# Performance work log

Hardware: AMD Instinct MI355X
Metric: run time of the kernel (lower is better)

Reference implementation:

```python
import jax, jax.numpy as jnp
import numpy as np

N = 50000
F_IN = 128
HID = 64
HEADS = 4
CLASSES = 16
E = 800000
NEG_SLOPE = 0.2


def _gat_layer(x, src, dst, W, a_src, a_dst, bias, heads, ch, concat):
    n = x.shape[0]
    h = (x @ W).reshape(n, heads, ch)                     # [N,H,C]
    alpha_src = jnp.einsum('nhc,hc->nh', h, a_src)        # [N,H]
    alpha_dst = jnp.einsum('nhc,hc->nh', h, a_dst)        # [N,H]
    e = jax.nn.leaky_relu(alpha_src[src] + alpha_dst[dst], NEG_SLOPE)  # [E,H]
    # segment softmax over edges grouped by destination node
    m = jax.ops.segment_max(e, dst, num_segments=n)       # [N,H]
    ex = jnp.exp(e - m[dst])                              # [E,H]
    s = jax.ops.segment_sum(ex, dst, num_segments=n)      # [N,H]
    alpha = ex / (s[dst] + 1e-16)                         # [E,H]
    # weighted scatter-add aggregation of neighbor features
    out = jax.ops.segment_sum(h[src] * alpha[:, :, None], dst, num_segments=n)  # [N,H,C]
    if concat:
        return out.reshape(n, heads * ch) + bias
    return out.mean(axis=1) + bias


def setup_inputs() -> dict:
    key = jax.random.key(0)
    ks = jax.random.split(key, 12)
    x = jax.random.normal(ks[0], (N, F_IN), dtype=jnp.float32)
    edge_index = jax.random.randint(ks[1], (2, E), 0, N, dtype=jnp.int64)
    g1 = 1.0 / np.sqrt(F_IN)
    g2 = 1.0 / np.sqrt(HID * HEADS)
    W1 = jax.random.normal(ks[2], (F_IN, HEADS * HID), dtype=jnp.float32) * g1
    a_src1 = jax.random.normal(ks[3], (HEADS, HID), dtype=jnp.float32) * g1
    a_dst1 = jax.random.normal(ks[4], (HEADS, HID), dtype=jnp.float32) * g1
    b1 = jnp.zeros((HEADS * HID,), dtype=jnp.float32)
    W2 = jax.random.normal(ks[5], (HEADS * HID, CLASSES), dtype=jnp.float32) * g2
    a_src2 = jax.random.normal(ks[6], (1, CLASSES), dtype=jnp.float32) * g2
    a_dst2 = jax.random.normal(ks[7], (1, CLASSES), dtype=jnp.float32) * g2
    b2 = jnp.zeros((CLASSES,), dtype=jnp.float32)
    return {"x": x, "edge_index": edge_index, "W1": W1, "a_src1": a_src1,
            "a_dst1": a_dst1, "b1": b1, "W2": W2, "a_src2": a_src2,
            "a_dst2": a_dst2, "b2": b2}


def reference(x, edge_index, W1, a_src1, a_dst1, b1, W2, a_src2, a_dst2, b2):
    n = x.shape[0]
    # add self-loops (PyG GATConv default add_self_loops=True)
    loops = jnp.arange(n, dtype=edge_index.dtype)
    src = jnp.concatenate([edge_index[0], loops])
    dst = jnp.concatenate([edge_index[1], loops])
    h = _gat_layer(x, src, dst, W1, a_src1, a_dst1, b1, HEADS, HID, concat=True)
    h = jax.nn.elu(h)
    out = _gat_layer(h, src, dst, W2, a_src2, a_dst2, b2, 1, CLASSES, concat=False)
    return jax.nn.log_softmax(out, axis=1)
```

## Files before the change

### kernel.cpp

```cpp
#include <hip/hip_runtime.h>
#include <hip/hip_fp16.h>
#include <math.h>

#define NEG 0.2f

typedef __attribute__((ext_vector_type(8))) short bf16x8;
typedef __attribute__((ext_vector_type(4))) float f32x4;

__device__ __forceinline__ float lrelu(float x){ return x > 0.f ? x : NEG*x; }

__device__ __forceinline__ float bflo(unsigned u){ return __uint_as_float(u << 16); }
__device__ __forceinline__ float bfhi(unsigned u){ return __uint_as_float(u & 0xffff0000u); }

__device__ __forceinline__ float selh(float a0, float a1, float a2, float a3,
                                      bool bit0, bool bit1){
  float lo = bit0 ? a1 : a0;
  float hi = bit0 ? a3 : a2;
  return bit1 ? hi : lo;
}

__device__ __forceinline__ unsigned short f2bf(float x){
  unsigned u = __float_as_uint(x);
  u += 0x7fffu + ((u >> 16) & 1u);
  return (unsigned short)(u >> 16);
}

#define FMA8(e, h) \
  acc[0]=fmaf(e,bflo(h.x),acc[0]); acc[1]=fmaf(e,bfhi(h.x),acc[1]); \
  acc[2]=fmaf(e,bflo(h.y),acc[2]); acc[3]=fmaf(e,bfhi(h.y),acc[3]); \
  acc[4]=fmaf(e,bflo(h.z),acc[4]); acc[5]=fmaf(e,bfhi(h.z),acc[5]); \
  acc[6]=fmaf(e,bflo(h.w),acc[6]); acc[7]=fmaf(e,bfhi(h.w),acc[7]);

__global__ void fill_kernel(const int* __restrict__ ei,
                            int* __restrict__ cnt, int* __restrict__ adj, int E){
  __shared__ int s_is64;
  if (threadIdx.x < 64){
    int v = ei[2*threadIdx.x + 1];
    unsigned long long b = __ballot(v != 0);
    if (threadIdx.x == 0) s_is64 = (b == 0ULL) ? 1 : 0;
  }
  __syncthreads();
  int is64 = s_is64;
  int stride = gridDim.x * blockDim.x;
  for (int i = blockIdx.x*blockDim.x + threadIdx.x; i < E; i += stride){
    int s = is64 ? ei[2*i]       : ei[i];
    int d = is64 ? ei[2*(E + i)] : ei[E + i];
    int pos = atomicAdd(&cnt[d], 1);
    if (pos < 64) adj[(d << 6) + pos] = s;
  }
}

__device__ __forceinline__ int wt_addr(int col, int k){
  int g = (k >> 3) ^ (col & 7);
  return col*128 + g*8 + (k & 7);
}

__global__ __launch_bounds__(256) void gemm1_mfma(const float* __restrict__ x,
                             const float* __restrict__ W,
                             const float* __restrict__ asrcw, const float* __restrict__ adstw,
                             unsigned short* __restrict__ h1b,
                             float* __restrict__ as1, float* __restrict__ ad1, int N){
  __shared__ unsigned short wt[256*128];
  int t = threadIdx.x;
  int lane = t & 63, w = t >> 6;
  int row0 = blockIdx.x * 64 + w * 16;

  int arow = row0 + (lane & 15);
  if (arow >= N) arow = N - 1;
  const float* xr = x + (size_t)arow * 128 + (lane >> 4) * 8;
  bf16x8 afrag[4];
  #pragma unroll
  for (int kk = 0; kk < 4; kk++){
    float4 p0 = *reinterpret_cast<const float4*>(xr + kk*32);
    float4 p1 = *reinterpret_cast<const float4*>(xr + kk*32 + 4);
    afrag[kk][0] = (short)f2bf(p0.x); afrag[kk][1] = (short)f2bf(p0.y);
    afrag[kk][2] = (short)f2bf(p0.z); afrag[kk][3] = (short)f2bf(p0.w);
    afrag[kk][4] = (short)f2bf(p1.x); afrag[kk][5] = (short)f2bf(p1.y);
    afrag[kk][6] = (short)f2bf(p1.z); afrag[kk][7] = (short)f2bf(p1.w);
  }

  int c = t;
  for (int k0 = 0; k0 < 128; k0 += 8){
    bf16x8 v;
    #pragma unroll
    for (int j = 0; j < 8; j++) v[j] = (short)f2bf(W[(size_t)(k0+j)*256 + c]);
    *reinterpret_cast<bf16x8*>(&wt[wt_addr(c, k0)]) = v;
  }
  __syncthreads();

  f32x4 acc[16];
  #pragma unroll
  for (int n = 0; n < 16; n++) acc[n] = (f32x4){0.f,0.f,0.f,0.f};
  #pragma unroll
  for (int kk = 0; kk < 4; kk++){
    #pragma unroll
    for (int n = 0; n < 16; n++){
      bf16x8 b = *reinterpret_cast<const bf16x8*>(
          &wt[wt_addr(n*16 + (lane & 15), kk*32 + (lane >> 4)*8)]);
      acc[n] = __builtin_amdgcn_mfma_f32_16x16x32_bf16(afrag[kk], b, acc[n], 0, 0, 0);
    }
  }

  int rbase = row0 + (lane >> 4)*4;
  int cbase = lane & 15;
  #pragma unroll
  for (int n = 0; n < 16; n++){
    #pragma unroll
    for (int r = 0; r < 4; r++){
      int row = rbase + r;
      if (row < N) h1b[(size_t)row*256 + n*16 + cbase] = f2bf(acc[n][r]);
    }
  }

  float av[16], dv[16];
  #pragma unroll
  for (int n = 0; n < 16; n++){
    av[n] = asrcw[n*16 + cbase];
    dv[n] = adstw[n*16 + cbase];
  }
  #pragma unroll
  for (int r = 0; r < 4; r++){
    int row = rbase + r;
    float hs[4], hd[4];
    #pragma unroll
    for (int h = 0; h < 4; h++){
      float ps = 0.f, pd = 0.f;
      #pragma unroll
      for (int q = 0; q < 4; q++){
        int n = h*4 + q;
        ps = fmaf(acc[n][r], av[n], ps);
        pd = fmaf(acc[n][r], dv[n], pd);
      }
      #pragma unroll
      for (int off = 1; off < 16; off <<= 1){
        ps += __shfl_xor(ps, off, 64);
        pd += __shfl_xor(pd, off, 64);
      }
      hs[h] = ps; hd[h] = pd;
    }
    if (cbase == 0 && row < N){
      *reinterpret_cast<float4*>(as1 + (size_t)row*4) = make_float4(hs[0],hs[1],hs[2],hs[3]);
      *reinterpret_cast<float4*>(ad1 + (size_t)row*4) = make_float4(hd[0],hd[1],hd[2],hd[3]);
    }
  }
}

__global__ void edge_exp_kernel(const float* __restrict__ as1, const float* __restrict__ ad1,
                                const int* __restrict__ cnt, const int* __restrict__ adj,
                                __half* __restrict__ exarr, float* __restrict__ den, int N){
  int node = (blockIdx.x*blockDim.x + threadIdx.x) >> 6;
  int lane = threadIdx.x & 63;
  if (node >= N) return;
  int cn = cnt[node]; if (cn > 64) cn = 64;
  int beg = node << 6;
  bool val = lane < cn;
  int src = val ? adj[beg + lane] : 0;
  float4 dv = *reinterpret_cast<const float4*>(ad1 + (size_t)node*4);
  float4 sv = *reinterpret_cast<const float4*>(as1 + (size_t)src*4);
  float ex0 = val ? __expf(lrelu(sv.x + dv.x)) : 0.f;
  float ex1 = val ? __expf(lrelu(sv.y + dv.y)) : 0.f;
  float ex2 = val ? __expf(lrelu(sv.z + dv.z)) : 0.f;
  float ex3 = val ? __expf(lrelu(sv.w + dv.w)) : 0.f;

  if (val){
    __half2 p0 = __floats2half2_rn(ex0, ex1);
    __half2 p1 = __floats2half2_rn(ex2, ex3);
    uint2 o;
    o.x = *reinterpret_cast<unsigned*>(&p0);
    o.y = *reinterpret_cast<unsigned*>(&p1);
    *reinterpret_cast<uint2*>(exarr + (size_t)(beg + lane)*4) = o;
  }

  float sp0 = ex0, sp1 = ex1, sp2 = ex2, sp3 = ex3;
  #pragma unroll
  for (int off = 32; off; off >>= 1){
    sp0 += __shfl_xor(sp0, off, 64);
    sp1 += __shfl_xor(sp1, off, 64);
    sp2 += __shfl_xor(sp2, off, 64);
    sp3 += __shfl_xor(sp3, off, 64);
  }
  float4 s2 = *reinterpret_cast<const float4*>(as1 + (size_t)node*4);
  float exs0 = __expf(lrelu(s2.x + dv.x));
  float exs1 = __expf(lrelu(s2.y + dv.y));
  float exs2 = __expf(lrelu(s2.z + dv.z));
  float exs3 = __expf(lrelu(s2.w + dv.w));
  if (lane == 0){
    *reinterpret_cast<float4*>(den + (size_t)node*8) =
        make_float4(sp0 + exs0, sp1 + exs1, sp2 + exs2, sp3 + exs3);
    *reinterpret_cast<float4*>(den + (size_t)node*8 + 4) =
        make_float4(exs0, exs1, exs2, exs3);
  }
}

__global__ void agg1_kernel(const unsigned short* __restrict__ h1b,
                            const float* __restrict__ b1,
                            const int* __restrict__ cnt, const int* __restrict__ adj,
                            const __half* __restrict__ exarr, const float* __restrict__ den,
                            unsigned short* __restrict__ hact_b, int N){
  int node = (blockIdx.x*blockDim.x + threadIdx.x) >> 6;
  int lane = threadIdx.x & 63;
  if (node >= N) return;
  int cn = cnt[node]; if (cn > 64) cn = 64;
  int beg = node << 6;
  int hf = lane >> 5;
  int sl = lane & 31;
  int hh = sl >> 3;
  bool hb0 = (sl & 8) != 0, hb1 = (sl & 16) != 0;
  const __half* exw = exarr + (size_t)beg*4;
  const int* aj = adj + beg;
  unsigned co = sl*8;

  float acc[8];
  #pragma unroll
  for (int q = 0; q < 8; q++) acc[q] = 0.f;

  int j = 0;
  for (; j + 8 <= cn; j += 8){
    int e0 = j+hf, e1 = j+2+hf, e2 = j+4+hf, e3 = j+6+hf;
    int s0 = aj[e0], s1 = aj[e1], s2 = aj[e2], s3 = aj[e3];
    float w0 = __half2float(exw[e0*4+hh]);
    float w1 = __half2float(exw[e1*4+hh]);
    float w2 = __half2float(exw[e2*4+hh]);
    float w3 = __half2float(exw[e3*4+hh]);
    uint4 h0 = *reinterpret_cast<const uint4*>(h1b + (size_t)s0*256 + co);
    uint4 h1 = *reinterpret_cast<const uint4*>(h1b + (size_t)s1*256 + co);
    uint4 h2 = *reinterpret_cast<const uint4*>(h1b + (size_t)s2*256 + co);
    uint4 h3 = *reinterpret_cast<const uint4*>(h1b + (size_t)s3*256 + co);
    FMA8(w0, h0); FMA8(w1, h1); FMA8(w2, h2); FMA8(w3, h3);
  }
  for (; j + 4 <= cn; j += 4){
    int e0 = j+hf, e1 = j+2+hf;
    int s0 = aj[e0], s1 = aj[e1];
    float w0 = __half2float(exw[e0*4+hh]);
    float w1 = __half2float(exw[e1*4+hh]);
    uint4 h0 = *reinterpret_cast<const uint4*>(h1b + (size_t)s0*256 + co);
    uint4 h1 = *reinterpret_cast<const uint4*>(h1b + (size_t)s1*256 + co);
    FMA8(w0, h0); FMA8(w1, h1);
  }
  for (; j < cn; j += 2){
    if (j + hf < cn){
      int e0 = j+hf;
      int s0 = aj[e0];
      float w0 = __half2float(exw[e0*4+hh]);
      uint4 h0 = *reinterpret_cast<const uint4*>(h1b + (size_t)s0*256 + co);
      FMA8(w0, h0);
    }
  }

  #pragma unroll
  for (int q = 0; q < 8; q++) acc[q] += __shfl_xor(acc[q], 32, 64);

  if (hf == 0){
    float4 dn  = *reinterpret_cast<const float4*>(den + (size_t)node*8);
    float4 dsf = *reinterpret_cast<const float4*>(den + (size_t)node*8 + 4);
    float dh  = selh(dn.x, dn.y, dn.z, dn.w, hb0, hb1);
    float ehs = selh(dsf.x, dsf.y, dsf.z, dsf.w, hb0, hb1);
    uint4 hv = *reinterpret_cast<const uint4*>(h1b + (size_t)node*256 + co);
    FMA8(ehs, hv);

    float rinv = 1.0f / (dh + 1e-16f);
    float4 bA = *reinterpret_cast<const float4*>(b1 + sl*8);
    float4 bB = *reinterpret_cast<const float4*>(b1 + sl*8 + 4);
    float o[8];
    o[0] = acc[0]*rinv + bA.x; o[1] = acc[1]*rinv + bA.y;
    o[2] = acc[2]*rinv + bA.z; o[3] = acc[3]*rinv + bA.w;
    o[4] = acc[4]*rinv + bB.x; o[5] = acc[5]*rinv + bB.y;
    o[6] = acc[6]*rinv + bB.z; o[7] = acc[7]*rinv + bB.w;
    #pragma unroll
    for (int q = 0; q < 8; q++) o[q] = o[q] > 0.f ? o[q] : expm1f(o[q]);
    uint4 ob;
    ob.x = (unsigned)f2bf(o[0]) | ((unsigned)f2bf(o[1]) << 16);
    ob.y = (unsigned)f2bf(o[2]) | ((unsigned)f2bf(o[3]) << 16);
    ob.z = (unsigned)f2bf(o[4]) | ((unsigned)f2bf(o[5]) << 16);
    ob.w = (unsigned)f2bf(o[6]) | ((unsigned)f2bf(o[7]) << 16);
    *reinterpret_cast<uint4*>(hact_b + (size_t)node*256 + co) = ob;
  }
}

__device__ __forceinline__ int wt2_addr(int col, int k){
  int g = (k >> 3) ^ (col & 7);
  return col*256 + g*8 + (k & 7);
}

__global__ __launch_bounds__(256) void gemm2_mfma(const unsigned short* __restrict__ hact_b,
                             const float* __restrict__ W2,
                             const float* __restrict__ asrc2, const float* __restrict__ adst2,
                             float* __restrict__ h2, float* __restrict__ as2,
                             float* __restrict__ ad2, int N){
  __shared__ unsigned short wt[16*256];
  int t = threadIdx.x;
  int lane = t & 63, w = t >> 6;
  int row0 = blockIdx.x * 64 + w * 16;

  {
    float4 r0 = *reinterpret_cast<const float4*>(W2 + (size_t)t*16);
    float4 r1 = *reinterpret_cast<const float4*>(W2 + (size_t)t*16 + 4);
    float4 r2 = *reinterpret_cast<const float4*>(W2 + (size_t)t*16 + 8);
    float4 r3 = *reinterpret_cast<const float4*>(W2 + (size_t)t*16 + 12);
    float wr[16] = {r0.x,r0.y,r0.z,r0.w, r1.x,r1.y,r1.z,r1.w,
                    r2.x,r2.y,r2.z,r2.w, r3.x,r3.y,r3.z,r3.w};
    #pragma unroll
    for (int cc = 0; cc < 16; cc++) wt[wt2_addr(cc, t)] = f2bf(wr[cc]);
  }

  int arow = row0 + (lane & 15);
  if (arow >= N) arow = N - 1;
  const unsigned short* hr = hact_b + (size_t)arow*256 + (lane >> 4)*8;
  __syncthreads();

  f32x4 acc = (f32x4){0.f,0.f,0.f,0.f};
  #pragma unroll
  for (int kk = 0; kk < 8; kk++){
    bf16x8 a = *reinterpret_cast<const bf16x8*>(hr + kk*32);
    bf16x8 b = *reinterpret_cast<const bf16x8*>(
        &wt[wt2_addr(lane & 15, kk*32 + (lane >> 4)*8)]);
    acc = __builtin_amdgcn_mfma_f32_16x16x32_bf16(a, b, acc, 0, 0, 0);
  }

  int rbase = row0 + (lane >> 4)*4;
  int cbase = lane & 15;
  float avc = asrc2[cbase], dvc = adst2[cbase];
  #pragma unroll
  for (int r = 0; r < 4; r++){
    int row = rbase + r;
    if (row < N) h2[(size_t)row*16 + cbase] = acc[r];
    float ps = acc[r]*avc, pd = acc[r]*dvc;
    #pragma unroll
    for (int off = 1; off < 16; off <<= 1){
      ps += __shfl_xor(ps, off, 64);
      pd += __shfl_xor(pd, off, 64);
    }
    if (cbase == 0 && row < N){ as2[row] = ps; ad2[row] = pd; }
  }
}

__global__ void agg2_kernel(const float* __restrict__ h2, const float* __restrict__ as2,
                            const float* __restrict__ ad2, const float* __restrict__ b2,
                            const int* __restrict__ cnt, const int* __restrict__ adj,
                            float* __restrict__ out, int N){
  int node = (blockIdx.x*blockDim.x + threadIdx.x) >> 6;
  int lane = threadIdx.x & 63;
  if (node >= N) return;
  int cn = cnt[node]; if (cn > 64) cn = 64;
  int beg = node << 6;
  int g = lane >> 4, c = lane & 15;

  bool val = lane < cn;
  int srcl = val ? adj[beg + lane] : 0;
  float adn = ad2[node];

  float v[16];
  #pragma unroll
  for (int q = 0; q < 16; q++){
    v[q] = 0.f;
    if (4*q < cn){
      int sj = __shfl(srcl, 4*q + g, 64);
      v[q] = h2[(size_t)sj*16 + c];
    }
  }

  float e = val ? lrelu(as2[srcl] + adn) : -3e38f;
  float ex = __expf(e);
  float sp = ex;
  #pragma unroll
  for (int off = 32; off; off >>= 1) sp += __shfl_xor(sp, off, 64);
  float eself = __expf(lrelu(as2[node] + adn));
  sp += eself;

  float acc = 0.f;
  #pragma unroll
  for (int q = 0; q < 16; q++){
    if (4*q < cn){
      float wj = __shfl(ex, 4*q + g, 64);
      acc = fmaf(wj, v[q], acc);
    }
  }
  acc += __shfl_xor(acc, 16, 64);
  acc += __shfl_xor(acc, 32, 64);

  if (g == 0){
    acc = fmaf(eself, h2[(size_t)node*16 + c], acc);
    float vv = acc / (sp + 1e-16f) + b2[c];
    float mx = vv;
    #pragma unroll
    for (int off = 1; off < 16; off <<= 1) mx = fmaxf(mx, __shfl_xor(mx, off, 64));
    float se = __expf(vv - mx);
    #pragma unroll
    for (int off = 1; off < 16; off <<= 1) se += __shfl_xor(se, off, 64);
    out[(size_t)node*16 + c] = vv - mx - logf(se);
  }
}

extern "C" void kernel_launch(void* const* d_in, const int* in_sizes, int n_in,
                              void* d_out, int out_size, void* d_ws, size_t ws_size,
                              hipStream_t stream){
  const float* x    = (const float*)d_in[0];
  const int*   ei   = (const int*)d_in[1];
  const float* W1   = (const float*)d_in[2];
  const float* as1w = (const float*)d_in[3];
  const float* ad1w = (const float*)d_in[4];
  const float* b1   = (const float*)d_in[5];
  const float* W2   = (const float*)d_in[6];
  const float* as2w = (const float*)d_in[7];
  const float* ad2w = (const float*)d_in[8];
  const float* b2   = (const float*)d_in[9];
  float* out = (float*)d_out;

  int N = in_sizes[0] / 128;
  int E = in_sizes[1] / 2;

  char* p = (char*)d_ws;
  size_t off = 0;
  auto alloc = [&](size_t b){ size_t c = off; off = (off + b + 255) & ~(size_t)255; return c; };
  unsigned short* h1b   = (unsigned short*)(p + alloc((size_t)N*256*2));
  unsigned short* hact_b= (unsigned short*)(p + alloc((size_t)N*256*2));
  float* h2     = (float*)(p + alloc((size_t)N*16*4));
  float* as1    = (float*)(p + alloc((size_t)N*4*4));
  float* ad1    = (float*)(p + alloc((size_t)N*4*4));
  float* as2    = (float*)(p + alloc((size_t)N*4));
  float* ad2    = (float*)(p + alloc((size_t)N*4));
  int*   cnt    = (int*)(p + alloc((size_t)N*4));
  int*   adj    = (int*)(p + alloc((size_t)N*64*4));
  __half* exarr = (__half*)(p + alloc((size_t)N*64*4*2));
  float* den    = (float*)(p + alloc((size_t)N*8*4));

  hipMemsetAsync(cnt, 0, (size_t)N*4, stream);
  fill_kernel<<<2048, 256, 0, stream>>>(ei, cnt, adj, E);

  gemm1_mfma<<<(N + 63)/64, 256, 0, stream>>>(x, W1, as1w, ad1w, h1b, as1, ad1, N);
  edge_exp_kernel<<<(N*64 + 255)/256, 256, 0, stream>>>(as1, ad1, cnt, adj, exarr, den, N);
  agg1_kernel<<<(N*64 + 255)/256, 256, 0, stream>>>(h1b, b1, cnt, adj, exarr, den, hact_b, N);
  gemm2_mfma<<<(N + 63)/64, 256, 0, stream>>>(hact_b, W2, as2w, ad2w, h2, as2, ad2, N);
  agg2_kernel<<<(N*64 + 255)/256, 256, 0, stream>>>(h2, as2, ad2, b2, cnt, adj, out, N);
}
```

Before: 190.9 us.

## Map two nodes per wavefront in agg1 instead of splitting edges across halves

The layer-1 aggregation kernel now gives each 32-lane half-wave its own destination node, so every half walks that node's full edge list. Previously both halves shared one node's edges and combined results with a cross-half shuffle. This removes that shuffle and the idle half during the epilogue, and halves the grid size. Other changes: 32-bit unsigned index math replaces size_t, and a fast __expf-1 replaces expm1f in the ELU. The risks are divergence between two nodes of different degree in one wave, a loss of ELU precision near zero, and possible overflow if the index math exceeds 32 bits.

Result: no change. 188.2 us (-1.4%).

```diff
diff --git a/kernel.cpp b/kernel.cpp
--- a/kernel.cpp
+++ b/kernel.cpp
@@ -197,84 +197,67 @@
                             const int* __restrict__ cnt, const int* __restrict__ adj,
                             const __half* __restrict__ exarr, const float* __restrict__ den,
                             unsigned short* __restrict__ hact_b, int N){
-  int node = (blockIdx.x*blockDim.x + threadIdx.x) >> 6;
+  int wid  = (blockIdx.x*blockDim.x + threadIdx.x) >> 6;
   int lane = threadIdx.x & 63;
+  int hf   = lane >> 5;
+  int node = (wid << 1) + hf;
   if (node >= N) return;
-  int cn = cnt[node]; if (cn > 64) cn = 64;
-  int beg = node << 6;
-  int hf = lane >> 5;
   int sl = lane & 31;
   int hh = sl >> 3;
   bool hb0 = (sl & 8) != 0, hb1 = (sl & 16) != 0;
-  const __half* exw = exarr + (size_t)beg*4;
+  int cn = cnt[node]; if (cn > 64) cn = 64;
+  unsigned beg = (unsigned)node << 6;
   const int* aj = adj + beg;
-  unsigned co = sl*8;
+  const __half* exw = exarr + ((size_t)beg * 4);
+  unsigned co = (unsigned)sl * 8;
 
   float acc[8];
   #pragma unroll
   for (int q = 0; q < 8; q++) acc[q] = 0.f;
 
   int j = 0;
-  for (; j + 8 <= cn; j += 8){
-    int e0 = j+hf, e1 = j+2+hf, e2 = j+4+hf, e3 = j+6+hf;
-    int s0 = aj[e0], s1 = aj[e1], s2 = aj[e2], s3 = aj[e3];
-    float w0 = __half2float(exw[e0*4+hh]);
-    float w1 = __half2float(exw[e1*4+hh]);
-    float w2 = __half2float(exw[e2*4+hh]);
-    float w3 = __half2float(exw[e3*4+hh]);
-    uint4 h0 = *reinterpret_cast<const uint4*>(h1b + (size_t)s0*256 + co);
-    uint4 h1 = *reinterpret_cast<const uint4*>(h1b + (size_t)s1*256 + co);
-    uint4 h2 = *reinterpret_cast<const uint4*>(h1b + (size_t)s2*256 + co);
-    uint4 h3 = *reinterpret_cast<const uint4*>(h1b + (size_t)s3*256 + co);
+  for (; j + 4 <= cn; j += 4){
+    int s0 = aj[j], s1 = aj[j+1], s2 = aj[j+2], s3 = aj[j+3];
+    float w0 = __half2float(exw[(unsigned)(j+0)*4 + hh]);
+    float w1 = __half2float(exw[(unsigned)(j+1)*4 + hh]);
+    float w2 = __half2float(exw[(unsigned)(j+2)*4 + hh]);
+    float w3 = __half2float(exw[(unsigned)(j+3)*4 + hh]);
+    uint4 h0 = *reinterpret_cast<const uint4*>(h1b + (((unsigned)s0 << 8) + co));
+    uint4 h1 = *reinterpret_cast<const uint4*>(h1b + (((unsigned)s1 << 8) + co));
+    uint4 h2 = *reinterpret_cast<const uint4*>(h1b + (((unsigned)s2 << 8) + co));
+    uint4 h3 = *reinterpret_cast<const uint4*>(h1b + (((unsigned)s3 << 8) + co));
     FMA8(w0, h0); FMA8(w1, h1); FMA8(w2, h2); FMA8(w3, h3);
   }
-  for (; j + 4 <= cn; j += 4){
-    int e0 = j+hf, e1 = j+2+hf;
-    int s0 = aj[e0], s1 = aj[e1];
-    float w0 = __half2float(exw[e0*4+hh]);
-    float w1 = __half2float(exw[e1*4+hh]);
-    uint4 h0 = *reinterpret_cast<const uint4*>(h1b + (size_t)s0*256 + co);
-    uint4 h1 = *reinterpret_cast<const uint4*>(h1b + (size_t)s1*256 + co);
-    FMA8(w0, h0); FMA8(w1, h1);
-  }
-  for (; j < cn; j += 2){
-    if (j + hf < cn){
-      int e0 = j+hf;
-      int s0 = aj[e0];
-      float w0 = __half2float(exw[e0*4+hh]);
-      uint4 h0 = *reinterpret_cast<const uint4*>(h1b + (size_t)s0*256 + co);
-      FMA8(w0, h0);
-    }
-  }
-
-  #pragma unroll
-  for (int q = 0; q < 8; q++) acc[q] += __shfl_xor(acc[q], 32, 64);
-
-  if (hf == 0){
-    float4 dn  = *reinterpret_cast<const float4*>(den + (size_t)node*8);
-    float4 dsf = *reinterpret_cast<const float4*>(den + (size_t)node*8 + 4);
-    float dh  = selh(dn.x, dn.y, dn.z, dn.w, hb0, hb1);
-    float ehs = selh(dsf.x, dsf.y, dsf.z, dsf.w, hb0, hb1);
-    uint4 hv = *reinterpret_cast<const uint4*>(h1b + (size_t)node*256 + co);
-    FMA8(ehs, hv);
-
-    float rinv = 1.0f / (dh + 1e-16f);
-    float4 bA = *reinterpret_cast<const float4*>(b1 + sl*8);
-    float4 bB = *reinterpret_cast<const float4*>(b1 + sl*8 + 4);
-    float o[8];
-    o[0] = acc[0]*rinv + bA.x; o[1] = acc[1]*rinv + bA.y;
-    o[2] = acc[2]*rinv + bA.z; o[3] = acc[3]*rinv + bA.w;
-    o[4] = acc[4]*rinv + bB.x; o[5] = acc[5]*rinv + bB.y;
-    o[6] = acc[6]*rinv + bB.z; o[7] = acc[7]*rinv + bB.w;
-    #pragma unroll
-    for (int q = 0; q < 8; q++) o[q] = o[q] > 0.f ? o[q] : expm1f(o[q]);
-    uint4 ob;
-    ob.x = (unsigned)f2bf(o[0]) | ((unsigned)f2bf(o[1]) << 16);
-    ob.y = (unsigned)f2bf(o[2]) | ((unsigned)f2bf(o[3]) << 16);
-    ob.z = (unsigned)f2bf(o[4]) | ((unsigned)f2bf(o[5]) << 16);
-    ob.w = (unsigned)f2bf(o[6]) | ((unsigned)f2bf(o[7]) << 16);
-    *reinterpret_cast<uint4*>(hact_b + (size_t)node*256 + co) = ob;
-  }
+  for (; j < cn; j++){
+    int s0 = aj[j];
+    float w0 = __half2float(exw[(unsigned)j*4 + hh]);
+    uint4 h0 = *reinterpret_cast<const uint4*>(h1b + (((unsigned)s0 << 8) + co));
+    FMA8(w0, h0);
+  }
+
+  float4 dn  = *reinterpret_cast<const float4*>(den + (size_t)node*8);
+  float4 dsf = *reinterpret_cast<const float4*>(den + (size_t)node*8 + 4);
+  float dh  = selh(dn.x, dn.y, dn.z, dn.w, hb0, hb1);
+  float ehs = selh(dsf.x, dsf.y, dsf.z, dsf.w, hb0, hb1);
+  uint4 hv = *reinterpret_cast<const uint4*>(h1b + (((unsigned)node << 8) + co));
+  FMA8(ehs, hv);
+
+  float rinv = 1.0f / (dh + 1e-16f);
+  float4 bA = *reinterpret_cast<const float4*>(b1 + co);
+  float4 bB = *reinterpret_cast<const float4*>(b1 + co + 4);
+  float o[8];
+  o[0] = acc[0]*rinv + bA.x; o[1] = acc[1]*rinv + bA.y;
+  o[2] = acc[2]*rinv + bA.z; o[3] = acc[3]*rinv + bA.w;
+  o[4] = acc[4]*rinv + bB.x; o[5] = acc[5]*rinv + bB.y;
+  o[6] = acc[6]*rinv + bB.z; o[7] = acc[7]*rinv + bB.w;
+  #pragma unroll
+  for (int q = 0; q < 8; q++) o[q] = o[q] > 0.f ? o[q] : (__expf(o[q]) - 1.f);
+  uint4 ob;
+  ob.x = (unsigned)f2bf(o[0]) | ((unsigned)f2bf(o[1]) << 16);
+  ob.y = (unsigned)f2bf(o[2]) | ((unsigned)f2bf(o[3]) << 16);
+  ob.z = (unsigned)f2bf(o[4]) | ((unsigned)f2bf(o[5]) << 16);
+  ob.w = (unsigned)f2bf(o[6]) | ((unsigned)f2bf(o[7]) << 16);
+  *reinterpret_cast<uint4*>(hact_b + (((unsigned)node << 8) + co)) = ob;
 }
 
 __device__ __forceinline__ int wt2_addr(int col, int k){
@@ -355,7 +338,7 @@
     v[q] = 0.f;
     if (4*q < cn){
       int sj = __shfl(srcl, 4*q + g, 64);
-      v[q] = h2[(size_t)sj*16 + c];
+      v[q] = h2[((unsigned)sj*16u + (unsigned)c)];
     }
   }
 
@@ -429,7 +412,7 @@
 
   gemm1_mfma<<<(N + 63)/64, 256, 0, stream>>>(x, W1, as1w, ad1w, h1b, as1, ad1, N);
   edge_exp_kernel<<<(N*64 + 255)/256, 256, 0, stream>>>(as1, ad1, cnt, adj, exarr, den, N);
-  agg1_kernel<<<(N*64 + 255)/256, 256, 0, stream>>>(h1b, b1, cnt, adj, exarr, den, hact_b, N);
+  agg1_kernel<<<(((N+1)/2)*64 + 255)/256, 256, 0, stream>>>(h1b, b1, cnt, adj, exarr, den, hact_b, N);
   gemm2_mfma<<<(N + 63)/64, 256, 0, stream>>>(hact_b, W2, as2w, ad2w, h2, as2, ad2, N);
   agg2_kernel<<<(N*64 + 255)/256, 256, 0, stream>>>(h2, as2, ad2, b2, cnt, adj, out, N);
 }
```
